# Performance work log

Hardware: AMD Instinct MI355X
Metric: run time of the kernel (lower is better)

Reference implementation:

```python
import jax, jax.numpy as jnp
import numpy as np


def _bicubic_warp(img, dx, dy):
    """Faithful JAX port of Warp_Object.forward with flag='bicubic'.
    img: [B,C,H,W] float32; dx, dy: [B,1,H,W] pixel displacements.
    Replicates the original tile-order quirk: X/Y are repeated C times along
    dim0 (order c*B+b) while the image is flattened in b*C+c order.
    """
    B, C, H, W = img.shape
    Wm1 = jnp.float32(max(W - 1, 1))
    Hm1 = jnp.float32(max(H - 1, 1))
    xs = jnp.arange(W, dtype=jnp.float32)
    ys = jnp.arange(H, dtype=jnp.float32)
    Xg, Yg = jnp.meshgrid(xs, ys)          # [H,W]
    # normalized grid in [-1,1] as in forward()
    newX = 2.0 * (Xg[None] + dx[:, 0]) / Wm1 - 1.0   # [B,H,W]
    newY = 2.0 * (Yg[None] + dy[:, 0]) / Hm1 - 1.0
    # repeat over channels exactly like X.repeat([C,1,1,1]) (tile order)
    x_map = (jnp.tile(newX, (C, 1, 1)) + 1.0) * Wm1 / 2.0   # [B*C,H,W]
    y_map = (jnp.tile(newY, (C, 1, 1)) + 1.0) * Hm1 / 2.0

    x0 = jnp.floor(x_map)
    y0 = jnp.floor(y_map)
    tx = x_map - x0
    ty = y_map - y0

    def cubic_coeffs(t):
        cm1 = (-t ** 3 + 2.0 * t ** 2 - t) / 2.0
        c0 = (3.0 * t ** 3 - 5.0 * t ** 2 + 2.0) / 2.0
        c1 = (-3.0 * t ** 3 + 4.0 * t ** 2 + t) / 2.0
        c2 = 1.0 - (cm1 + c0 + c1)
        return (cm1, c0, c1, c2)

    cx = cubic_coeffs(tx)
    cy = cubic_coeffs(ty)

    x0i = x0.astype(jnp.int32)
    y0i = y0.astype(jnp.int32)
    xi = [jnp.clip(x0i + o, 0, W - 1) for o in (-1, 0, 1, 2)]
    yi = [jnp.clip(y0i + o, 0, H - 1) for o in (-1, 0, 1, 2)]

    flat = img.reshape(B * C, H, W)
    row = jnp.arange(B * C)[:, None, None]   # per-image base offset

    out = jnp.zeros_like(x_map)
    for j in range(4):            # 4 rows of the 4x4 bicubic stencil
        row_acc = jnp.zeros_like(x_map)
        for i in range(4):
            row_acc = row_acc + cx[i] * flat[row, yi[j], xi[i]]
        out = out + cy[j] * row_acc
    return out.reshape(B, C, H, W)


def setup_inputs() -> dict:
    key = jax.random.key(0)
    k1, k2, k3 = jax.random.split(key, 3)
    B, C, H, W = 4, 3, 512, 512
    input_image = jax.random.normal(k1, (B, C, H, W), dtype=jnp.float32)
    delta_x = jax.random.normal(k2, (B, 1, H, W), dtype=jnp.float32) * 1.5
    delta_y = jax.random.normal(k3, (B, 1, H, W), dtype=jnp.float32) * 1.5
    return {"input_image": input_image, "delta_x": delta_x, "delta_y": delta_y}


def reference(input_image, delta_x, delta_y):
    return _bicubic_warp(input_image, delta_x, delta_y)
```

## Files before the change

### kernel.cpp

```cpp
#include <hip/hip_runtime.h>


constexpr int B = 4, C = 3, H = 512, W = 512;
constexpr int HW = H * W;
constexpr int TS = 32;
constexpr int HALO = 6;
constexpr int RS = TS + 2 * HALO;
constexpr int LSTC = 48;
constexpr int CHR = LSTC / 4;
constexpr int NCH = RS * CHR;
constexpr int CPW = NCH / 16;
constexpr int TDW = RS * LSTC;
constexpr int NT = 1024;
constexpr int NB = 512;

typedef float f4 __attribute__((ext_vector_type(4)));
typedef f4 f4u __attribute__((aligned(4)));

typedef const __attribute__((address_space(1))) void* gas_t;
typedef __attribute__((address_space(3))) void* las_t;

__device__ __forceinline__ void gload_lds16(const float* g, float* l) {
    __builtin_amdgcn_global_load_lds((gas_t)g, (las_t)l, 16, 0, 0);
}

struct Coef {
    float w0, w1, w2, w3;
    float cy0, cy1, cy2, cy3;
    int   lbase;
    bool  intile;
    int   y0, s;
};

__device__ __forceinline__ Coef make_coef(int x, int y, float dxv, float dyv,
                                          int yb, int cb) {
    Coef cf;
    float xm = (float)x + dxv;
    float ym = (float)y + dyv;
    float x0f = floorf(xm), y0f = floorf(ym);
    float ftx = xm - x0f, fty = ym - y0f;
    int x0 = (int)x0f, y0 = (int)y0f;
    int s  = min(max(x0 - 1, 0), W - 4);

    float tx2 = ftx * ftx, tx3 = tx2 * ftx;
    float cx0 = (-tx3 + 2.0f * tx2 - ftx) * 0.5f;
    float cx1 = (3.0f * tx3 - 5.0f * tx2 + 2.0f) * 0.5f;
    float cx2 = (-tx3 * 3.0f + 4.0f * tx2 + ftx) * 0.5f;
    float cx3 = 1.0f - (cx0 + cx1 + cx2);

    float ty2 = fty * fty, ty3 = ty2 * fty;
    cf.cy0 = (-ty3 + 2.0f * ty2 - fty) * 0.5f;
    cf.cy1 = (3.0f * ty3 - 5.0f * ty2 + 2.0f) * 0.5f;
    cf.cy2 = (-3.0f * ty3 + 4.0f * ty2 + fty) * 0.5f;
    cf.cy3 = 1.0f - (cf.cy0 + cf.cy1 + cf.cy2);

    if (__builtin_expect(x0 >= 1 && x0 <= W - 3, 1)) {
        cf.w0 = cx0; cf.w1 = cx1; cf.w2 = cx2; cf.w3 = cx3;
    } else {
        float w0 = 0.f, w1 = 0.f, w2 = 0.f, w3 = 0.f;
        const float cxa[4] = {cx0, cx1, cx2, cx3};
#pragma unroll
        for (int o = 0; o < 4; ++o) {
            int xi = min(max(x0 - 1 + o, 0), W - 1);
            int e  = xi - s;
            float cc = cxa[o];
            w0 += (e == 0) ? cc : 0.f;
            w1 += (e == 1) ? cc : 0.f;
            w2 += (e == 2) ? cc : 0.f;
            w3 += (e == 3) ? cc : 0.f;
        }
        cf.w0 = w0; cf.w1 = w1; cf.w2 = w2; cf.w3 = w3;
    }

    unsigned rel = (unsigned)(y0 - (yb - HALO + 1));
    unsigned lsv = (unsigned)(s - cb);
    cf.intile = (rel <= (unsigned)(RS - 4)) & (lsv <= (unsigned)(LSTC - 4));
    cf.lbase  = (int)rel * LSTC + (int)lsv;
    cf.y0 = y0; cf.s = s;
    return cf;
}

__device__ __forceinline__ float stencil1(const float* __restrict__ tp,
                                          const Coef& cf,
                                          const float* __restrict__ plane) {
    if (__builtin_expect(cf.intile, 1)) {
        const float* rp = tp + cf.lbase;
        float r0 = cf.cy0 * (cf.w0 * rp[0] + cf.w1 * rp[1] + cf.w2 * rp[2] + cf.w3 * rp[3]);
        rp += LSTC;
        float r1 = cf.cy1 * (cf.w0 * rp[0] + cf.w1 * rp[1] + cf.w2 * rp[2] + cf.w3 * rp[3]);
        rp += LSTC;
        float r2 = cf.cy2 * (cf.w0 * rp[0] + cf.w1 * rp[1] + cf.w2 * rp[2] + cf.w3 * rp[3]);
        rp += LSTC;
        float r3 = cf.cy3 * (cf.w0 * rp[0] + cf.w1 * rp[1] + cf.w2 * rp[2] + cf.w3 * rp[3]);
        return (r0 + r1) + (r2 + r3);
    } else {
        const float cya[4] = {cf.cy0, cf.cy1, cf.cy2, cf.cy3};
        float acc = 0.f;
#pragma unroll
        for (int j = 0; j < 4; ++j) {
            int yi = min(max(cf.y0 - 1 + j, 0), H - 1);
            f4 v = *(const f4u*)(plane + yi * W + cf.s);
            acc += cya[j] * (cf.w0 * v.x + cf.w1 * v.y + cf.w2 * v.z + cf.w3 * v.w);
        }
        return acc;
    }
}

__device__ __forceinline__ void stage_tile(const float* __restrict__ img, int bd,
                                           int yb, int cb, float* dst,
                                           int wv, int lane) {
    if (lane < CPW) {
        int chunk = wv * CPW + lane;
        int r  = chunk / CHR;
        int c4 = (chunk - r * CHR) * 4;
        int sr = min(max(yb - HALO + r, 0), H - 1);
        int soff = sr * W + cb + c4;
        const float* g0 = img + (size_t)bd * HW + soff;
        float* l0 = dst + chunk * 4;
        gload_lds16(g0,          l0);
        gload_lds16(g0 + 4 * HW, l0 + TDW);
        gload_lds16(g0 + 8 * HW, l0 + 2 * TDW);
    }
}

__global__ __launch_bounds__(NT, 8)
void warp_bicubic_2t(const float* __restrict__ img,
                     const float* __restrict__ dxp,
                     const float* __restrict__ dyp,
                     float* __restrict__ out)
{
    __shared__ float tile[2][C * TDW];

    int b   = blockIdx.x;
    int swz = (b & 7) * (NB / 8) + (b >> 3);
    int bd  = swz >> 7;
    int rem = swz & 127;
    int typ = rem >> 4;
    int txx = rem & 15;
    int xb  = txx * TS;
    int cb  = min(max(xb - HALO, 0), W - LSTC);
    int yb0 = typ * 2 * TS;
    int yb1 = yb0 + TS;

    int tid  = threadIdx.x;
    int wv   = tid >> 6;
    int lane = tid & 63;
    int ry   = wv * 2 + (lane >> 5);
    int cidx = lane & 31;
    int x    = xb + cidx;
    int po0  = (yb0 + ry) * W + x;
    int po1  = (yb1 + ry) * W + x;

    float dx0 = __builtin_nontemporal_load(dxp + bd * HW + po0);
    float dy0 = __builtin_nontemporal_load(dyp + bd * HW + po0);
    float dx1 = __builtin_nontemporal_load(dxp + bd * HW + po1);
    float dy1 = __builtin_nontemporal_load(dyp + bd * HW + po1);

    Coef c0 = make_coef(x, yb0 + ry, dx0, dy0, yb0, cb);
    Coef c1 = make_coef(x, yb1 + ry, dx1, dy1, yb1, cb);
    __builtin_amdgcn_sched_barrier(0);

    stage_tile(img, bd, yb0, cb, &tile[0][0], wv, lane);
    __builtin_amdgcn_sched_barrier(0);
    stage_tile(img, bd, yb1, cb, &tile[1][0], wv, lane);
    __builtin_amdgcn_sched_barrier(0);

    asm volatile("s_waitcnt vmcnt(3)" ::: "memory");
    __builtin_amdgcn_sched_barrier(0);
    __builtin_amdgcn_s_barrier();

#pragma unroll
    for (int c = 0; c < C; ++c) {
        int kp = bd + 4 * c;
        float acc = stencil1(&tile[0][c * TDW], c0, img + (size_t)kp * HW);
        __builtin_nontemporal_store(acc, out + (size_t)kp * HW + po0);
    }

    asm volatile("s_waitcnt vmcnt(3)" ::: "memory");
    __builtin_amdgcn_sched_barrier(0);
    __builtin_amdgcn_s_barrier();

#pragma unroll
    for (int c = 0; c < C; ++c) {
        int kp = bd + 4 * c;
        float acc = stencil1(&tile[1][c * TDW], c1, img + (size_t)kp * HW);
        __builtin_nontemporal_store(acc, out + (size_t)kp * HW + po1);
    }
}

extern "C" void kernel_launch(void* const* d_in, const int* in_sizes, int n_in,
                              void* d_out, int out_size, void* d_ws, size_t ws_size,
                              hipStream_t stream) {
    const float* img = (const float*)d_in[0];
    const float* dx  = (const float*)d_in[1];
    const float* dy  = (const float*)d_in[2];
    float* out = (float*)d_out;

    dim3 block(NT);
    dim3 grid(NB);
    hipLaunchKernelGGL(warp_bicubic_2t, grid, block, 0, stream,
                       img, dx, dy, out);
}
```

Before: 16.74 us.

## Process vertical strips of four tiles per block with double-buffered LDS

New measurement: 18.05 us. 1.08x slower.

```diff
diff --git a/kernel.cpp b/kernel.cpp
--- a/kernel.cpp
+++ b/kernel.cpp
@@ -4,6 +4,7 @@
 constexpr int B = 4, C = 3, H = 512, W = 512;
 constexpr int HW = H * W;
 constexpr int TS = 32;
+constexpr int NTILE = 4;
 constexpr int HALO = 6;
 constexpr int RS = TS + 2 * HALO;
 constexpr int LSTC = 48;
@@ -12,7 +13,7 @@
 constexpr int CPW = NCH / 16;
 constexpr int TDW = RS * LSTC;
 constexpr int NT = 1024;
-constexpr int NB = 512;
+constexpr int NB = 256;
 
 typedef float f4 __attribute__((ext_vector_type(4)));
 typedef f4 f4u __attribute__((aligned(4)));
@@ -45,7 +46,7 @@
     float tx2 = ftx * ftx, tx3 = tx2 * ftx;
     float cx0 = (-tx3 + 2.0f * tx2 - ftx) * 0.5f;
     float cx1 = (3.0f * tx3 - 5.0f * tx2 + 2.0f) * 0.5f;
-    float cx2 = (-tx3 * 3.0f + 4.0f * tx2 + ftx) * 0.5f;
+    float cx2 = (-3.0f * tx3 + 4.0f * tx2 + ftx) * 0.5f;
     float cx3 = 1.0f - (cx0 + cx1 + cx2);
 
     float ty2 = fty * fty, ty3 = ty2 * fty;
@@ -123,68 +124,74 @@
     }
 }
 
-__global__ __launch_bounds__(NT, 8)
-void warp_bicubic_2t(const float* __restrict__ img,
-                     const float* __restrict__ dxp,
-                     const float* __restrict__ dyp,
-                     float* __restrict__ out)
+__global__ __launch_bounds__(NT, 4)
+void warp_bicubic_strip(const float* __restrict__ img,
+                        const float* __restrict__ dxp,
+                        const float* __restrict__ dyp,
+                        float* __restrict__ out)
 {
     __shared__ float tile[2][C * TDW];
 
     int b   = blockIdx.x;
     int swz = (b & 7) * (NB / 8) + (b >> 3);
-    int bd  = swz >> 7;
-    int rem = swz & 127;
-    int typ = rem >> 4;
-    int txx = rem & 15;
-    int xb  = txx * TS;
-    int cb  = min(max(xb - HALO, 0), W - LSTC);
-    int yb0 = typ * 2 * TS;
-    int yb1 = yb0 + TS;
+    int bd   = swz >> 6;
+    int rem  = swz & 63;
+    int sc   = rem & 15;
+    int srow = rem >> 4;
+    int xb   = sc * TS;
+    int cb   = min(max(xb - HALO, 0), W - LSTC);
+    int yb0  = srow * (NTILE * TS);
 
     int tid  = threadIdx.x;
     int wv   = tid >> 6;
     int lane = tid & 63;
     int ry   = wv * 2 + (lane >> 5);
-    int cidx = lane & 31;
-    int x    = xb + cidx;
-    int po0  = (yb0 + ry) * W + x;
-    int po1  = (yb1 + ry) * W + x;
-
-    float dx0 = __builtin_nontemporal_load(dxp + bd * HW + po0);
-    float dy0 = __builtin_nontemporal_load(dyp + bd * HW + po0);
-    float dx1 = __builtin_nontemporal_load(dxp + bd * HW + po1);
-    float dy1 = __builtin_nontemporal_load(dyp + bd * HW + po1);
-
-    Coef c0 = make_coef(x, yb0 + ry, dx0, dy0, yb0, cb);
-    Coef c1 = make_coef(x, yb1 + ry, dx1, dy1, yb1, cb);
-    __builtin_amdgcn_sched_barrier(0);
-
-    stage_tile(img, bd, yb0, cb, &tile[0][0], wv, lane);
-    __builtin_amdgcn_sched_barrier(0);
-    stage_tile(img, bd, yb1, cb, &tile[1][0], wv, lane);
-    __builtin_amdgcn_sched_barrier(0);
-
-    asm volatile("s_waitcnt vmcnt(3)" ::: "memory");
-    __builtin_amdgcn_sched_barrier(0);
-    __builtin_amdgcn_s_barrier();
-
-#pragma unroll
-    for (int c = 0; c < C; ++c) {
-        int kp = bd + 4 * c;
-        float acc = stencil1(&tile[0][c * TDW], c0, img + (size_t)kp * HW);
-        __builtin_nontemporal_store(acc, out + (size_t)kp * HW + po0);
-    }
-
-    asm volatile("s_waitcnt vmcnt(3)" ::: "memory");
-    __builtin_amdgcn_sched_barrier(0);
-    __builtin_amdgcn_s_barrier();
-
-#pragma unroll
-    for (int c = 0; c < C; ++c) {
-        int kp = bd + 4 * c;
-        float acc = stencil1(&tile[1][c * TDW], c1, img + (size_t)kp * HW);
-        __builtin_nontemporal_store(acc, out + (size_t)kp * HW + po1);
+    int x    = xb + (lane & 31);
+
+    {
+        int po = (yb0 + ry) * W + x;
+        float dxv = __builtin_nontemporal_load(dxp + bd * HW + po);
+        float dyv = __builtin_nontemporal_load(dyp + bd * HW + po);
+        stage_tile(img, bd, yb0, cb, &tile[0][0], wv, lane);
+        Coef cf = make_coef(x, yb0 + ry, dxv, dyv, yb0, cb);
+
+        asm volatile("s_waitcnt vmcnt(0)" ::: "memory");
+        __builtin_amdgcn_sched_barrier(0);
+        __builtin_amdgcn_s_barrier();
+        __builtin_amdgcn_sched_barrier(0);
+
+#pragma unroll
+        for (int t = 0; t < NTILE; ++t) {
+            int yb  = yb0 + t * TS;
+            int poT = (yb + ry) * W + x;
+
+            float dxn = 0.f, dyn = 0.f;
+            if (t + 1 < NTILE) {
+                int poN = (yb + TS + ry) * W + x;
+                dxn = __builtin_nontemporal_load(dxp + bd * HW + poN);
+                dyn = __builtin_nontemporal_load(dyp + bd * HW + poN);
+                stage_tile(img, bd, yb + TS, cb, &tile[(t + 1) & 1][0], wv, lane);
+            }
+            __builtin_amdgcn_sched_barrier(0);
+
+#pragma unroll
+            for (int c = 0; c < C; ++c) {
+                int kp = bd + 4 * c;
+                float acc = stencil1(&tile[t & 1][c * TDW], cf,
+                                     img + (size_t)kp * HW);
+                __builtin_nontemporal_store(acc, out + (size_t)kp * HW + poT);
+            }
+            __builtin_amdgcn_sched_barrier(0);
+
+            if (t + 1 < NTILE) {
+                Coef cfN = make_coef(x, yb + TS + ry, dxn, dyn, yb + TS, cb);
+                asm volatile("s_waitcnt vmcnt(3)" ::: "memory");
+                __builtin_amdgcn_sched_barrier(0);
+                __builtin_amdgcn_s_barrier();
+                __builtin_amdgcn_sched_barrier(0);
+                cf = cfN;
+            }
+        }
     }
 }
 
@@ -198,6 +205,6 @@
 
     dim3 block(NT);
     dim3 grid(NB);
-    hipLaunchKernelGGL(warp_bicubic_2t, grid, block, 0, stream,
+    hipLaunchKernelGGL(warp_bicubic_strip, grid, block, 0, stream,
                        img, dx, dy, out);
 }
```
